# Kernel tuning notes

Hardware: AMD Instinct MI355X
Metric: run time of the kernel (lower is better)

The kernel has to match this reference:

```python
import math
import jax, jax.numpy as jnp
import numpy as np

B, T, C = 2, 2048, 2048
H, G = 16, 4
D = C // H  # head_dim = 128
KV = G * D
SOFT_CAP = 50.0
EPS = 1e-6


def setup_inputs() -> dict:
    key = jax.random.key(0)
    ks = jax.random.split(key, 5)
    s = 1.0 / math.sqrt(C)
    return {
        "x": jax.random.normal(ks[0], (B, T, C), jnp.float32),
        "Wq": jax.random.normal(ks[1], (C, C), jnp.float32) * s,
        "Wk": jax.random.normal(ks[2], (KV, C), jnp.float32) * s,
        "Wv": jax.random.normal(ks[3], (KV, C), jnp.float32) * s,
        "Wo": jax.random.normal(ks[4], (C, C), jnp.float32) * s,
        "bo": jnp.zeros((C,), jnp.float32),
        "q_norm_w": jnp.ones((D,), jnp.float32),
        "k_norm_w": jnp.ones((D,), jnp.float32),
    }


def _rmsnorm(x, w):
    # norm/sqrt(d) formulation, eps added to rms (matches torch module exactly)
    rms = jnp.linalg.norm(x, axis=-1, keepdims=True) / math.sqrt(x.shape[-1])
    return w * (x / (rms + EPS))


def _rotary_tables(seq_len, dim):
    inv_freq = 1.0 / (10000.0 ** (jnp.arange(0, dim, 2, dtype=jnp.float32) / dim))
    t = jnp.arange(seq_len, dtype=jnp.float32)
    freqs = jnp.outer(t, inv_freq)  # [T, D/2]
    return jnp.cos(freqs), jnp.sin(freqs)


def _apply_rope(x, cos, sin):
    # x: [B, T, h, D]; cos/sin: [T, D/2] broadcast as [1, T, 1, D/2]
    d = x.shape[-1] // 2
    x1, x2 = x[..., :d], x[..., d:]
    c = cos[None, :, None, :]
    s = sin[None, :, None, :]
    return jnp.concatenate([x1 * c + x2 * s, -x1 * s + x2 * c], axis=-1)


def reference(x, Wq, Wk, Wv, Wo, bo, q_norm_w, k_norm_w):
    b, t, c = x.shape
    q = (x @ Wq.T).reshape(b, t, H, D)
    k = (x @ Wk.T).reshape(b, t, G, D)
    v = (x @ Wv.T).reshape(b, t, G, D)

    cos, sin = _rotary_tables(t, D)
    q = _apply_rope(_rmsnorm(q, q_norm_w), cos, sin)
    k = _apply_rope(_rmsnorm(k, k_norm_w), cos, sin)

    q = q.transpose(0, 2, 1, 3)              # [B, H, T, D]
    k = jnp.repeat(k.transpose(0, 2, 1, 3), H // G, axis=1)  # [B, H, T, D]
    v = jnp.repeat(v.transpose(0, 2, 1, 3), H // G, axis=1)

    att = jnp.einsum("bhqd,bhkd->bhqk", q, k) / math.sqrt(D)
    causal = jnp.tril(jnp.ones((t, t), bool))
    att = jnp.where(causal[None, None], att, -jnp.inf)
    att = SOFT_CAP * jnp.tanh(att / SOFT_CAP)  # masked entries -> -50
    att = jax.nn.softmax(att, axis=-1)

    y = jnp.einsum("bhqk,bhkd->bhqd", att, v)
    y = y.transpose(0, 2, 1, 3).reshape(b, t, c)
    return y @ Wo.T + bo
```

## Files before the change

kernel.cpp:

```cpp
#include <hip/hip_runtime.h>
#include <math.h>

#define T_SEQ 2048
#define C_DIM 2048
#define NH    16
#define NG    4
#define DH    128
#define BATCH 2

typedef unsigned short u16;
typedef __bf16 bf16_t;
typedef bf16_t bf16x8 __attribute__((ext_vector_type(8)));
typedef float  f32x4  __attribute__((ext_vector_type(4)));

static __device__ __forceinline__ u16 f2bf(float f) {
    return __builtin_bit_cast(u16, (__bf16)f);
}

static __device__ __forceinline__ void gll16(const void* g, void* lds) {
    __builtin_amdgcn_global_load_lds(
        (const __attribute__((address_space(1))) void*)(unsigned long long)(g),
        (__attribute__((address_space(3))) void*)(unsigned int)(unsigned long long)(lds),
        16, 0, 0);
}

__global__ __launch_bounds__(256)
void cast_multi(const float* __restrict__ x,  const float* __restrict__ wq,
                const float* __restrict__ wk, const float* __restrict__ wv,
                u16* __restrict__ xo, u16* __restrict__ wqo,
                u16* __restrict__ wko, u16* __restrict__ wvo) {
    int i = blockIdx.x * 256 + threadIdx.x;
    const float* src; u16* dst; int off;
    if (i < 1048576)      { src = x;  dst = xo;  off = i; }
    else if (i < 1572864) { src = wq; dst = wqo; off = i - 1048576; }
    else if (i < 1703936) { src = wk; dst = wko; off = i - 1572864; }
    else                  { src = wv; dst = wvo; off = i - 1703936; }
    const float4* p = (const float4*)src + (size_t)off * 2;
    float4 a = p[0], b = p[1];
    u16 u[8] = {f2bf(a.x), f2bf(a.y), f2bf(a.z), f2bf(a.w),
                f2bf(b.x), f2bf(b.y), f2bf(b.z), f2bf(b.w)};
    *(uint4*)(dst + (size_t)off * 8) = *(const uint4*)u;
}

__global__ __launch_bounds__(256)
void cast_f32_bf16(const float* __restrict__ in, u16* __restrict__ out, int n8) {
    int i = blockIdx.x * 256 + threadIdx.x;
    if (i >= n8) return;
    const float4* p = (const float4*)in + (size_t)i * 2;
    float4 a = p[0], b = p[1];
    u16 u[8] = {f2bf(a.x), f2bf(a.y), f2bf(a.z), f2bf(a.w),
                f2bf(b.x), f2bf(b.y), f2bf(b.z), f2bf(b.w)};
    *(uint4*)(out + (size_t)i * 8) = *(const uint4*)u;
}

static __device__ __forceinline__ void gemm_body(
        u16* As, u16* Bs,
        const u16* __restrict__ A, const u16* __restrict__ B,
        const float* __restrict__ bias, float* __restrict__ C,
        int N, int K, int m0, int n0) {
    const int t    = threadIdx.x;
    const int lane = t & 63, w = t >> 6;
    const int l15  = lane & 15, quad = lane >> 4;
    const int wr   = w >> 1, wc = w & 1;

    f32x4 acc[4][4];
#pragma unroll
    for (int mt = 0; mt < 4; ++mt)
#pragma unroll
        for (int nt = 0; nt < 4; ++nt) acc[mt][nt] = (f32x4){0.f, 0.f, 0.f, 0.f};

    const int off0 = w*2048 + lane*16;
    const int r0 = off0 >> 6,          c0 = (off0 & 63) >> 1;
    const int r1 = (off0+1024) >> 6,   c1 = ((off0+1024) & 63) >> 1;
    const u16* Ag0 = A + (size_t)(m0 + r0) * K + c0;
    const u16* Ag1 = A + (size_t)(m0 + r1) * K + c1;
    const u16* Bg0 = B + (size_t)(n0 + r0) * K + c0;
    const u16* Bg1 = B + (size_t)(n0 + r1) * K + c1;
    char* AsB = (char*)As; char* BsB = (char*)Bs;
    const int ldsOff0 = w*2048, ldsOff1 = w*2048 + 1024;

    for (int k0 = 0; k0 < K; k0 += 32) {
        gll16(Ag0 + k0, AsB + ldsOff0);
        gll16(Ag1 + k0, AsB + ldsOff1);
        gll16(Bg0 + k0, BsB + ldsOff0);
        gll16(Bg1 + k0, BsB + ldsOff1);
        __syncthreads();
        bf16x8 af[4], bf[4];
#pragma unroll
        for (int mt = 0; mt < 4; ++mt)
            af[mt] = __builtin_bit_cast(bf16x8,
                *(const uint4*)&As[(wr*64 + mt*16 + l15)*32 + quad*8]);
#pragma unroll
        for (int nt = 0; nt < 4; ++nt)
            bf[nt] = __builtin_bit_cast(bf16x8,
                *(const uint4*)&Bs[(wc*64 + nt*16 + l15)*32 + quad*8]);
#pragma unroll
        for (int mt = 0; mt < 4; ++mt)
#pragma unroll
            for (int nt = 0; nt < 4; ++nt)
                acc[mt][nt] = __builtin_amdgcn_mfma_f32_16x16x32_bf16(
                                  af[mt], bf[nt], acc[mt][nt], 0, 0, 0);
        __syncthreads();
    }

#pragma unroll
    for (int mt = 0; mt < 4; ++mt)
#pragma unroll
        for (int nt = 0; nt < 4; ++nt) {
            const int col = n0 + wc*64 + nt*16 + l15;
            const float bv = bias ? bias[col] : 0.f;
#pragma unroll
            for (int r = 0; r < 4; ++r) {
                const int row = m0 + wr*64 + mt*16 + quad*4 + r;
                C[(size_t)row * N + col] = acc[mt][nt][r] + bv;
            }
        }
}

__global__ __launch_bounds__(256)
void gemm_nt_bf16(const u16* __restrict__ A, const u16* __restrict__ B,
                  const float* __restrict__ bias, float* __restrict__ C,
                  int N, int K) {
    __shared__ __align__(16) u16 As[128*32];
    __shared__ __align__(16) u16 Bs[128*32];
    gemm_body(As, Bs, A, B, bias, C, N, K, blockIdx.y*128, blockIdx.x*128);
}

__global__ __launch_bounds__(256)
void gemm_qkv(const u16* __restrict__ A,  const u16* __restrict__ Bq,
              const u16* __restrict__ Bk, const u16* __restrict__ Bv,
              float* __restrict__ Cq, float* __restrict__ Ck, float* __restrict__ Cv) {
    __shared__ __align__(16) u16 As[128*32];
    __shared__ __align__(16) u16 Bs[128*32];
    const int bx = blockIdx.x;
    const u16* B; float* C; int N, n0;
    if (bx < 16)      { B = Bq; C = Cq; N = 2048; n0 = bx * 128; }
    else if (bx < 20) { B = Bk; C = Ck; N = 512;  n0 = (bx-16) * 128; }
    else              { B = Bv; C = Cv; N = 512;  n0 = (bx-20) * 128; }
    gemm_body(As, Bs, A, B, nullptr, C, N, 2048, blockIdx.y*128, n0);
}

__global__ __launch_bounds__(256)
void rmsnorm_rope_qk(const float* __restrict__ qf, const float* __restrict__ kf,
                     const float* __restrict__ qw, const float* __restrict__ kw,
                     u16* __restrict__ qo, u16* __restrict__ ko) {
    const int blk  = blockIdx.x;
    const int sub  = threadIdx.x >> 6;
    const int lane = threadIdx.x & 63;
    const float* in; const float* w; u16* out; int row, nheads; float scale;
    if (blk < 16384) {
        in = qf; w = qw; out = qo; nheads = NH; scale = 0.08838834764831845f;
        row = blk * 4 + sub;
    } else {
        in = kf; w = kw; out = ko; nheads = NG; scale = 1.0f;
        row = (blk - 16384) * 4 + sub;
    }
    const float* p = in + (size_t)row * 128;
    float x1 = p[lane], x2 = p[lane + 64];
    float ss = x1*x1 + x2*x2;
#pragma unroll
    for (int off = 32; off >= 1; off >>= 1) ss += __shfl_xor(ss, off, 64);
    float inv = 1.0f / (sqrtf(ss * (1.0f/128.0f)) + 1e-6f);
    float x1n = w[lane]      * x1 * inv;
    float x2n = w[lane + 64] * x2 * inv;
    int tpos = (row / nheads) & (T_SEQ - 1);
    float invfreq = powf(10000.0f, -(float)lane / 64.0f);
    float s, c;
    sincosf((float)tpos * invfreq, &s, &c);
    out[(size_t)row*128 + lane]      = f2bf((x1n * c + x2n * s) * scale);
    out[(size_t)row*128 + lane + 64] = f2bf((x2n * c - x1n * s) * scale);
}

__global__ __launch_bounds__(256)
void v_cast_transpose(const float* __restrict__ v, u16* __restrict__ vt) {
    __shared__ u16 Lt[128 * 66];
    const int t  = threadIdx.x;
    const int t0 = blockIdx.x * 64;
    const int bg = blockIdx.y;
    const int b  = bg / NG, g = bg % NG;
#pragma unroll
    for (int rep = 0; rep < 8; ++rep) {
        int idx = rep * 256 + t;
        int i   = idx >> 5;
        int c   = idx & 31;
        float4 f = *(const float4*)(v + ((size_t)(b*T_SEQ + t0 + i)*NG + g)*DH + c*4);
        Lt[(c*4+0)*66 + i] = f2bf(f.x);
        Lt[(c*4+1)*66 + i] = f2bf(f.y);
        Lt[(c*4+2)*66 + i] = f2bf(f.z);
        Lt[(c*4+3)*66 + i] = f2bf(f.w);
    }
    __syncthreads();
#pragma unroll
    for (int rep = 0; rep < 4; ++rep) {
        int idx = rep * 256 + t;
        int d = idx >> 3, c = idx & 7;
        const u16* src = &Lt[d*66 + c*8];
        uint4 val;
        val.x = *(const unsigned int*)(src + 0);
        val.y = *(const unsigned int*)(src + 2);
        val.z = *(const unsigned int*)(src + 4);
        val.w = *(const unsigned int*)(src + 6);
        *(uint4*)(vt + ((size_t)(bg*DH + d))*T_SEQ + t0 + c*8) = val;
    }
}

__global__ __launch_bounds__(256, 2)
void flash_attn_mfma(const u16* __restrict__ qh, const u16* __restrict__ kh,
                     const u16* __restrict__ vt, u16* __restrict__ y) {
    __shared__ __align__(16) u16 Ks[2][64*128];
    __shared__ __align__(16) u16 Vs[2][128*64];
    __shared__ __align__(16) u16 Ps[64*64];

    const int t    = threadIdx.x;
    const int lane = t & 63, w = t >> 6;
    const int l15  = lane & 15, quad = lane >> 4;
    const int bg   = blockIdx.y;
    const int b    = bg >> 2, g = bg & 3;
    const int chunk = b ? (int)blockIdx.x : (63 - (int)blockIdx.x);
    const int q0   = chunk * 32;
    const int h    = g * (NH / NG) + w;

    const float L2E = 1.4426950408889634f;

    bf16x8 aq[2][4];
#pragma unroll
    for (int m = 0; m < 2; ++m) {
        const u16* qp = qh + ((size_t)(b*T_SEQ + q0 + m*16 + l15) * NH + h) * DH;
#pragma unroll
        for (int kc = 0; kc < 4; ++kc)
            aq[m][kc] = __builtin_bit_cast(bf16x8, *(const uint4*)(qp + kc*32 + quad*8));
    }

    f32x4 accO[2][8];
#pragma unroll
    for (int m = 0; m < 2; ++m)
#pragma unroll
        for (int nd = 0; nd < 8; ++nd) accO[m][nd] = (f32x4){0.f, 0.f, 0.f, 0.f};
    float ls[2][4] = {{0.f,0.f,0.f,0.f},{0.f,0.f,0.f,0.f}};

    const u16* kgb = kh + ((size_t)b*T_SEQ*NG + g)*DH;
    const u16* vgb = vt + ((size_t)(b*NG + g)*DH)*T_SEQ;

    const int krb = t >> 4, kcl = t & 15;
    const int vdb = t >> 3, vcl = t & 7;

    const int ktiles = q0/64 + 1;

#pragma unroll
    for (int j = 0; j < 4; ++j) {
        const int kr = j*16 + krb;
        gll16(kgb + (size_t)kr*(NG*DH) + ((kcl ^ (kr & 7)) << 3),
              (char*)Ks[0] + j*4096 + w*1024);
        const int vd = j*32 + vdb;
        gll16(vgb + (size_t)vd*T_SEQ + ((vcl ^ (vd & 7)) << 3),
              (char*)Vs[0] + j*4096 + w*1024);
    }

    for (int kt = 0; kt < ktiles; ++kt) {
        asm volatile("s_waitcnt vmcnt(0)" ::: "memory");
        __syncthreads();

        if (kt + 1 < ktiles) {
            const int k0n = (kt + 1) * 64, bn = (kt + 1) & 1;
#pragma unroll
            for (int j = 0; j < 4; ++j) {
                const int kr = j*16 + krb;
                gll16(kgb + (size_t)(k0n + kr)*(NG*DH) + ((kcl ^ (kr & 7)) << 3),
                      (char*)Ks[bn] + j*4096 + w*1024);
                const int vd = j*32 + vdb;
                gll16(vgb + (size_t)vd*T_SEQ + k0n + ((vcl ^ (vd & 7)) << 3),
                      (char*)Vs[bn] + j*4096 + w*1024);
            }
        }

        const u16* Kb = Ks[kt & 1];
        const u16* Vb = Vs[kt & 1];
        const int k0 = kt * 64;

        f32x4 accS[2][4];
#pragma unroll
        for (int m = 0; m < 2; ++m)
#pragma unroll
            for (int nt = 0; nt < 4; ++nt) accS[m][nt] = (f32x4){0.f,0.f,0.f,0.f};

#pragma unroll
        for (int nt = 0; nt < 4; ++nt) {
            const int krow = nt*16 + l15;
            const int kswz = (krow & 7) << 3;
#pragma unroll
            for (int kc = 0; kc < 4; ++kc) {
                bf16x8 bk = __builtin_bit_cast(bf16x8,
                    *(const uint4*)&Kb[krow*128 + ((kc*32 + quad*8) ^ kswz)]);
                accS[0][nt] = __builtin_amdgcn_mfma_f32_16x16x32_bf16(aq[0][kc], bk, accS[0][nt], 0, 0, 0);
                accS[1][nt] = __builtin_amdgcn_mfma_f32_16x16x32_bf16(aq[1][kc], bk, accS[1][nt], 0, 0, 0);
            }
        }

        bf16x8 ap[2][2];
#pragma unroll
        for (int m = 0; m < 2; ++m) {
#pragma unroll
            for (int nt = 0; nt < 4; ++nt) {
                const int colg = k0 + nt*16 + l15;
#pragma unroll
                for (int r = 0; r < 4; ++r) {
                    const int rowg = q0 + m*16 + quad*4 + r;
                    float s = accS[m][nt][r];
                    float z = s * 0.02f;
                    float u = z * z;
                    float poly = fmaf(u, fmaf(u, fmaf(u, -0.05396825396825397f,
                                           0.13333333333333333f),
                                          -0.3333333333333333f), 1.0f);
                    float p = __builtin_amdgcn_exp2f(s * poly * L2E);
                    p = (colg > rowg) ? 0.f : p;
                    ls[m][r] += p;
                    const int prow = w*16 + quad*4 + r;
                    Ps[prow*64 + ((nt*16 + l15) ^ ((prow & 7) << 3))] = f2bf(p);
                }
            }
            const int arow = w*16 + l15;
            const int aswz = (arow & 7) << 3;
            ap[m][0] = __builtin_bit_cast(bf16x8,
                *(const uint4*)&Ps[arow*64 + ((quad*8)      ^ aswz)]);
            ap[m][1] = __builtin_bit_cast(bf16x8,
                *(const uint4*)&Ps[arow*64 + ((32 + quad*8) ^ aswz)]);
        }

#pragma unroll
        for (int nd = 0; nd < 8; ++nd) {
            const int vrow = nd*16 + l15;
            const int vswz = (vrow & 7) << 3;
#pragma unroll
            for (int kc = 0; kc < 2; ++kc) {
                bf16x8 bv = __builtin_bit_cast(bf16x8,
                    *(const uint4*)&Vb[vrow*64 + ((kc*32 + quad*8) ^ vswz)]);
                accO[0][nd] = __builtin_amdgcn_mfma_f32_16x16x32_bf16(ap[0][kc], bv, accO[0][nd], 0, 0, 0);
                accO[1][nd] = __builtin_amdgcn_mfma_f32_16x16x32_bf16(ap[1][kc], bv, accO[1][nd], 0, 0, 0);
            }
        }
    }

#pragma unroll
    for (int m = 0; m < 2; ++m)
#pragma unroll
        for (int r = 0; r < 4; ++r) {
            float v = ls[m][r];
            v += __shfl_xor(v, 1, 64);
            v += __shfl_xor(v, 2, 64);
            v += __shfl_xor(v, 4, 64);
            v += __shfl_xor(v, 8, 64);
            const float invl = 1.f / v;
            u16* yp = y + (size_t)(b*T_SEQ + q0 + m*16 + quad*4 + r) * C_DIM + h*DH;
#pragma unroll
            for (int nd = 0; nd < 8; ++nd)
                yp[nd*16 + l15] = f2bf(accO[m][nd][r] * invl);
        }
}

extern "C" void kernel_launch(void* const* d_in, const int* in_sizes, int n_in,
                              void* d_out, int out_size, void* d_ws, size_t ws_size,
                              hipStream_t stream) {
    const float* x  = (const float*)d_in[0];
    const float* Wq = (const float*)d_in[1];
    const float* Wk = (const float*)d_in[2];
    const float* Wv = (const float*)d_in[3];
    const float* Wo = (const float*)d_in[4];
    const float* bo = (const float*)d_in[5];
    const float* qw = (const float*)d_in[6];
    const float* kw = (const float*)d_in[7];
    float* out = (float*)d_out;

    const size_t qE = (size_t)BATCH * T_SEQ * NH * DH;
    const size_t kE = (size_t)BATCH * T_SEQ * NG * DH;
    const size_t wqE = (size_t)C_DIM * C_DIM;

    float* qf  = (float*)d_ws;
    float* kf  = qf + qE;
    float* vf  = kf + kE;
    u16*   qh  = (u16*)(vf + kE);
    u16*   khb = qh + qE;
    u16*   vtb = khb + kE;
    u16*   xh  = vtb + kE;
    u16*   wqh = xh + qE;
    u16*   wkh = wqh + wqE;
    u16*   wvh = wkh + (size_t)(NG*DH)*C_DIM;
    u16*   woh = (u16*)kf;
    u16*   yh  = (u16*)qf;

    const int M = BATCH * T_SEQ;
    dim3 blk(256);

    cast_multi<<<dim3(7168), blk, 0, stream>>>(x, Wq, Wk, Wv, xh, wqh, wkh, wvh);

    gemm_qkv<<<dim3(24, M/128), blk, 0, stream>>>(xh, wqh, wkh, wvh, qf, kf, vf);

    rmsnorm_rope_qk<<<dim3(M*NH/4 + M*NG/4), blk, 0, stream>>>(qf, kf, qw, kw, qh, khb);
    v_cast_transpose<<<dim3(T_SEQ/64, BATCH*NG), blk, 0, stream>>>(vf, vtb);

    cast_f32_bf16<<<dim3(wqE/8/256), blk, 0, stream>>>(Wo, woh, wqE/8);

    flash_attn_mfma<<<dim3(T_SEQ/32, BATCH*NG), dim3(256), 0, stream>>>(qh, khb, vtb, yh);

    gemm_nt_bf16<<<dim3(C_DIM/128, M/128), blk, 0, stream>>>(yh, woh, bo, out, C_DIM, C_DIM);
}
```

Before: 343.2 us.

## Split KV tiles across two wave groups in flash attention with LDS reduction

The attention block doubles to 512 threads. Two sets of four waves each process alternating 64-key tiles (even and odd), and their partial outputs and row sums are merged through shared memory at the end. The loop also drops cross-iteration double buffering: both tiles are loaded and then synchronised each pair. The causal mask now runs only on the diagonal tile, the log2e factor is folded into the polynomial, and MFMA phases are wrapped in s_setprio. This adds intra-block KV parallelism at the cost of extra LDS, a final reduction, and exposed load latency.

Measured after the change: 481.6 us. +40.3%, slower.

```diff
diff --git a/kernel.cpp b/kernel.cpp
--- a/kernel.cpp
+++ b/kernel.cpp
@@ -204,23 +204,28 @@
     }
 }
 
-__global__ __launch_bounds__(256, 2)
+__global__ __launch_bounds__(512, 4)
 void flash_attn_mfma(const u16* __restrict__ qh, const u16* __restrict__ kh,
                      const u16* __restrict__ vt, u16* __restrict__ y) {
-    __shared__ __align__(16) u16 Ks[2][64*128];
-    __shared__ __align__(16) u16 Vs[2][128*64];
-    __shared__ __align__(16) u16 Ps[64*64];
+    __shared__ __align__(16) u16 smem[40960];
+    u16* Ks = smem;
+    u16* Vs = smem + 16384;
+    u16* Ps = smem + 32768;
 
     const int t    = threadIdx.x;
     const int lane = t & 63, w = t >> 6;
+    const int h4   = w & 3,  s = w >> 2;
     const int l15  = lane & 15, quad = lane >> 4;
     const int bg   = blockIdx.y;
     const int b    = bg >> 2, g = bg & 3;
     const int chunk = b ? (int)blockIdx.x : (63 - (int)blockIdx.x);
     const int q0   = chunk * 32;
-    const int h    = g * (NH / NG) + w;
-
-    const float L2E = 1.4426950408889634f;
+    const int h    = g * (NH / NG) + h4;
+
+    const float C0 =  1.4426950408889634f;
+    const float C1 = -0.48089834696298777f;
+    const float C2 =  0.19235933878519512f;
+    const float C3 = -0.07785972536301652f;
 
     bf16x8 aq[2][4];
 #pragma unroll
@@ -245,116 +250,157 @@
     const int vdb = t >> 3, vcl = t & 7;
 
     const int ktiles = q0/64 + 1;
-
-#pragma unroll
-    for (int j = 0; j < 4; ++j) {
-        const int kr = j*16 + krb;
-        gll16(kgb + (size_t)kr*(NG*DH) + ((kcl ^ (kr & 7)) << 3),
-              (char*)Ks[0] + j*4096 + w*1024);
-        const int vd = j*32 + vdb;
-        gll16(vgb + (size_t)vd*T_SEQ + ((vcl ^ (vd & 7)) << 3),
-              (char*)Vs[0] + j*4096 + w*1024);
-    }
-
-    for (int kt = 0; kt < ktiles; ++kt) {
+    const int npairs = (ktiles + 1) >> 1;
+
+    for (int p = 0; p < npairs; ++p) {
+        {
+            const int k0e = 2*p*64;
+#pragma unroll
+            for (int j = 0; j < 2; ++j) {
+                const int kr = j*32 + krb;
+                gll16(kgb + (size_t)(k0e + kr)*(NG*DH) + ((kcl ^ (kr & 7)) << 3),
+                      (char*)Ks + j*8192 + w*1024);
+                const int vd = j*64 + vdb;
+                gll16(vgb + (size_t)vd*T_SEQ + k0e + ((vcl ^ (vd & 7)) << 3),
+                      (char*)Vs + j*8192 + w*1024);
+            }
+        }
+        if (2*p + 1 < ktiles) {
+            const int k0o = (2*p + 1)*64;
+#pragma unroll
+            for (int j = 0; j < 2; ++j) {
+                const int kr = j*32 + krb;
+                gll16(kgb + (size_t)(k0o + kr)*(NG*DH) + ((kcl ^ (kr & 7)) << 3),
+                      (char*)Ks + 16384 + j*8192 + w*1024);
+                const int vd = j*64 + vdb;
+                gll16(vgb + (size_t)vd*T_SEQ + k0o + ((vcl ^ (vd & 7)) << 3),
+                      (char*)Vs + 16384 + j*8192 + w*1024);
+            }
+        }
         asm volatile("s_waitcnt vmcnt(0)" ::: "memory");
         __syncthreads();
 
-        if (kt + 1 < ktiles) {
-            const int k0n = (kt + 1) * 64, bn = (kt + 1) & 1;
-#pragma unroll
-            for (int j = 0; j < 4; ++j) {
-                const int kr = j*16 + krb;
-                gll16(kgb + (size_t)(k0n + kr)*(NG*DH) + ((kcl ^ (kr & 7)) << 3),
-                      (char*)Ks[bn] + j*4096 + w*1024);
-                const int vd = j*32 + vdb;
-                gll16(vgb + (size_t)vd*T_SEQ + k0n + ((vcl ^ (vd & 7)) << 3),
-                      (char*)Vs[bn] + j*4096 + w*1024);
-            }
-        }
-
-        const u16* Kb = Ks[kt & 1];
-        const u16* Vb = Vs[kt & 1];
-        const int k0 = kt * 64;
-
-        f32x4 accS[2][4];
+        const int kt = 2*p + s;
+        if (kt < ktiles) {
+            const u16* Kb = Ks + s*8192;
+            const u16* Vb = Vs + s*8192;
+            const int k0 = kt * 64;
+            const bool diag = (kt == ktiles - 1);
+
+            f32x4 accS[2][4];
+#pragma unroll
+            for (int m = 0; m < 2; ++m)
+#pragma unroll
+                for (int nt = 0; nt < 4; ++nt) accS[m][nt] = (f32x4){0.f,0.f,0.f,0.f};
+
+            __builtin_amdgcn_s_setprio(1);
+#pragma unroll
+            for (int nt = 0; nt < 4; ++nt) {
+                const int krow = nt*16 + l15;
+                const int kswz = (krow & 7) << 3;
+#pragma unroll
+                for (int kc = 0; kc < 4; ++kc) {
+                    bf16x8 bk = __builtin_bit_cast(bf16x8,
+                        *(const uint4*)&Kb[krow*128 + ((kc*32 + quad*8) ^ kswz)]);
+                    accS[0][nt] = __builtin_amdgcn_mfma_f32_16x16x32_bf16(aq[0][kc], bk, accS[0][nt], 0, 0, 0);
+                    accS[1][nt] = __builtin_amdgcn_mfma_f32_16x16x32_bf16(aq[1][kc], bk, accS[1][nt], 0, 0, 0);
+                }
+            }
+            __builtin_amdgcn_s_setprio(0);
+
+            bf16x8 ap[2][2];
+#pragma unroll
+            for (int m = 0; m < 2; ++m) {
+#pragma unroll
+                for (int nt = 0; nt < 4; ++nt) {
+                    const int colg = k0 + nt*16 + l15;
+#pragma unroll
+                    for (int r = 0; r < 4; ++r) {
+                        float sv = accS[m][nt][r];
+                        float z = sv * 0.02f;
+                        float u = z * z;
+                        float poly = fmaf(u, fmaf(u, fmaf(u, C3, C2), C1), C0);
+                        float pv = __builtin_amdgcn_exp2f(sv * poly);
+                        if (diag) {
+                            const int rowg = q0 + m*16 + quad*4 + r;
+                            pv = (colg > rowg) ? 0.f : pv;
+                        }
+                        ls[m][r] += pv;
+                        const int prow = w*16 + r*4 + quad;
+                        const int pswz = ((quad << 1) | (r & 1)) << 3;
+                        Ps[prow*64 + ((nt*16 + l15) ^ pswz)] = f2bf(pv);
+                    }
+                }
+                const int srow = (l15 & 3)*4 + (l15 >> 2);
+                const int arow = w*16 + srow;
+                const int aswz = (((l15 >> 2) << 1) | (l15 & 1)) << 3;
+                ap[m][0] = __builtin_bit_cast(bf16x8,
+                    *(const uint4*)&Ps[arow*64 + ((quad*8)      ^ aswz)]);
+                ap[m][1] = __builtin_bit_cast(bf16x8,
+                    *(const uint4*)&Ps[arow*64 + ((32 + quad*8) ^ aswz)]);
+            }
+
+            __builtin_amdgcn_s_setprio(1);
+#pragma unroll
+            for (int nd = 0; nd < 8; ++nd) {
+                const int vrow = nd*16 + l15;
+                const int vswz = (vrow & 7) << 3;
+#pragma unroll
+                for (int kc = 0; kc < 2; ++kc) {
+                    bf16x8 bv = __builtin_bit_cast(bf16x8,
+                        *(const uint4*)&Vb[vrow*64 + ((kc*32 + quad*8) ^ vswz)]);
+                    accO[0][nd] = __builtin_amdgcn_mfma_f32_16x16x32_bf16(ap[0][kc], bv, accO[0][nd], 0, 0, 0);
+                    accO[1][nd] = __builtin_amdgcn_mfma_f32_16x16x32_bf16(ap[1][kc], bv, accO[1][nd], 0, 0, 0);
+                }
+            }
+            __builtin_amdgcn_s_setprio(0);
+        }
+        __syncthreads();
+    }
+
+    if (s == 1) {
+        float* od = (float*)smem + h4*4096;
+        float* ld = (float*)smem + 16384 + h4*512;
+#pragma unroll
+        for (int m = 0; m < 2; ++m) {
+#pragma unroll
+            for (int nd = 0; nd < 8; ++nd)
+                *(f32x4*)(od + (m*8 + nd)*256 + lane*4) = accO[m][nd];
+#pragma unroll
+            for (int r = 0; r < 4; ++r)
+                ld[(m*4 + r)*64 + lane] = ls[m][r];
+        }
+    }
+    __syncthreads();
+    if (s == 0) {
+        const float* od = (const float*)smem + h4*4096;
+        const float* ld = (const float*)smem + 16384 + h4*512;
+#pragma unroll
+        for (int m = 0; m < 2; ++m) {
+#pragma unroll
+            for (int nd = 0; nd < 8; ++nd)
+                accO[m][nd] += *(const f32x4*)(od + (m*8 + nd)*256 + lane*4);
+#pragma unroll
+            for (int r = 0; r < 4; ++r)
+                ls[m][r] += ld[(m*4 + r)*64 + lane];
+        }
+
 #pragma unroll
         for (int m = 0; m < 2; ++m)
 #pragma unroll
-            for (int nt = 0; nt < 4; ++nt) accS[m][nt] = (f32x4){0.f,0.f,0.f,0.f};
-
-#pragma unroll
-        for (int nt = 0; nt < 4; ++nt) {
-            const int krow = nt*16 + l15;
-            const int kswz = (krow & 7) << 3;
-#pragma unroll
-            for (int kc = 0; kc < 4; ++kc) {
-                bf16x8 bk = __builtin_bit_cast(bf16x8,
-                    *(const uint4*)&Kb[krow*128 + ((kc*32 + quad*8) ^ kswz)]);
-                accS[0][nt] = __builtin_amdgcn_mfma_f32_16x16x32_bf16(aq[0][kc], bk, accS[0][nt], 0, 0, 0);
-                accS[1][nt] = __builtin_amdgcn_mfma_f32_16x16x32_bf16(aq[1][kc], bk, accS[1][nt], 0, 0, 0);
-            }
-        }
-
-        bf16x8 ap[2][2];
-#pragma unroll
-        for (int m = 0; m < 2; ++m) {
-#pragma unroll
-            for (int nt = 0; nt < 4; ++nt) {
-                const int colg = k0 + nt*16 + l15;
-#pragma unroll
-                for (int r = 0; r < 4; ++r) {
-                    const int rowg = q0 + m*16 + quad*4 + r;
-                    float s = accS[m][nt][r];
-                    float z = s * 0.02f;
-                    float u = z * z;
-                    float poly = fmaf(u, fmaf(u, fmaf(u, -0.05396825396825397f,
-                                           0.13333333333333333f),
-                                          -0.3333333333333333f), 1.0f);
-                    float p = __builtin_amdgcn_exp2f(s * poly * L2E);
-                    p = (colg > rowg) ? 0.f : p;
-                    ls[m][r] += p;
-                    const int prow = w*16 + quad*4 + r;
-                    Ps[prow*64 + ((nt*16 + l15) ^ ((prow & 7) << 3))] = f2bf(p);
-                }
-            }
-            const int arow = w*16 + l15;
-            const int aswz = (arow & 7) << 3;
-            ap[m][0] = __builtin_bit_cast(bf16x8,
-                *(const uint4*)&Ps[arow*64 + ((quad*8)      ^ aswz)]);
-            ap[m][1] = __builtin_bit_cast(bf16x8,
-                *(const uint4*)&Ps[arow*64 + ((32 + quad*8) ^ aswz)]);
-        }
-
-#pragma unroll
-        for (int nd = 0; nd < 8; ++nd) {
-            const int vrow = nd*16 + l15;
-            const int vswz = (vrow & 7) << 3;
-#pragma unroll
-            for (int kc = 0; kc < 2; ++kc) {
-                bf16x8 bv = __builtin_bit_cast(bf16x8,
-                    *(const uint4*)&Vb[vrow*64 + ((kc*32 + quad*8) ^ vswz)]);
-                accO[0][nd] = __builtin_amdgcn_mfma_f32_16x16x32_bf16(ap[0][kc], bv, accO[0][nd], 0, 0, 0);
-                accO[1][nd] = __builtin_amdgcn_mfma_f32_16x16x32_bf16(ap[1][kc], bv, accO[1][nd], 0, 0, 0);
-            }
-        }
-    }
-
-#pragma unroll
-    for (int m = 0; m < 2; ++m)
-#pragma unroll
-        for (int r = 0; r < 4; ++r) {
-            float v = ls[m][r];
-            v += __shfl_xor(v, 1, 64);
-            v += __shfl_xor(v, 2, 64);
-            v += __shfl_xor(v, 4, 64);
-            v += __shfl_xor(v, 8, 64);
-            const float invl = 1.f / v;
-            u16* yp = y + (size_t)(b*T_SEQ + q0 + m*16 + quad*4 + r) * C_DIM + h*DH;
-#pragma unroll
-            for (int nd = 0; nd < 8; ++nd)
-                yp[nd*16 + l15] = f2bf(accO[m][nd][r] * invl);
-        }
+            for (int r = 0; r < 4; ++r) {
+                float v = ls[m][r];
+                v += __shfl_xor(v, 1, 64);
+                v += __shfl_xor(v, 2, 64);
+                v += __shfl_xor(v, 4, 64);
+                v += __shfl_xor(v, 8, 64);
+                const float invl = 1.f / v;
+                u16* yp = y + (size_t)(b*T_SEQ + q0 + m*16 + quad*4 + r) * C_DIM + h*DH;
+#pragma unroll
+                for (int nd = 0; nd < 8; ++nd)
+                    yp[nd*16 + l15] = f2bf(accO[m][nd][r] * invl);
+            }
+    }
 }
 
 extern "C" void kernel_launch(void* const* d_in, const int* in_sizes, int n_in,
@@ -399,7 +445,7 @@
 
     cast_f32_bf16<<<dim3(wqE/8/256), blk, 0, stream>>>(Wo, woh, wqE/8);
 
-    flash_attn_mfma<<<dim3(T_SEQ/32, BATCH*NG), dim3(256), 0, stream>>>(qh, khb, vtb, yh);
+    flash_attn_mfma<<<dim3(T_SEQ/32, BATCH*NG), dim3(512), 0, stream>>>(qh, khb, vtb, yh);
 
     gemm_nt_bf16<<<dim3(C_DIM/128, M/128), blk, 0, stream>>>(yh, woh, bo, out, C_DIM, C_DIM);
 }
```
